# Kernel tuning notes

Measured on AMD Instinct MI355X. Metric: run time of the kernel, lower is better.

Reference implementation:

```python
import jax, jax.numpy as jnp
import numpy as np

C = 256      # in_channels
CI = 128     # inter_channels = in_channels // 2
B, H, W = 16, 64, 64
EPS = 1e-5   # BatchNorm2d default eps


def conv1x1(x, w, b=None):
    # x: (b,c,h,w), w: (o,c) -> (b,o,h,w)
    out = jnp.einsum('bchw,oc->bohw', x, w)
    if b is not None:
        out = out + b[None, :, None, None]
    return out


def maxpool2x2(x):
    b, c, h, w = x.shape
    return x.reshape(b, c, h // 2, 2, w // 2, 2).max(axis=(3, 5))


def setup_inputs() -> dict:
    key = jax.random.key(0)
    ks = jax.random.split(key, 12)
    s_in = 1.0 / np.sqrt(C)
    s_int = 1.0 / np.sqrt(CI)
    return {
        'x': jax.random.normal(ks[0], (B, C, H, W), jnp.float32),
        'y': jax.random.normal(ks[1], (B, C, H, W), jnp.float32),
        'theta_w': jax.random.uniform(ks[2], (CI, C), jnp.float32, -s_in, s_in),
        'theta_b': jax.random.uniform(ks[3], (CI,), jnp.float32, -s_in, s_in),
        'phi_w': jax.random.uniform(ks[4], (CI, C), jnp.float32, -s_in, s_in),
        'phi_b': jax.random.uniform(ks[5], (CI,), jnp.float32, -s_in, s_in),
        'g_w': jax.random.uniform(ks[6], (CI, C), jnp.float32, -s_in, s_in),
        'g_b': jax.random.uniform(ks[7], (CI,), jnp.float32, -s_in, s_in),
        'W_w': jax.random.uniform(ks[8], (C, CI), jnp.float32, -s_int, s_int),
        'W_b': jax.random.uniform(ks[9], (C,), jnp.float32, -s_int, s_int),
        'bn_gamma': jax.random.normal(ks[10], (C,), jnp.float32) * 0.1,
        'bn_beta': jax.random.normal(ks[11], (C,), jnp.float32) * 0.1,
    }


def reference(x, y, theta_w, theta_b, phi_w, phi_b, g_w, g_b, W_w, W_b, bn_gamma, bn_beta):
    b, c, h, w = x.shape
    # g branch: 1x1 conv on y + 2x2 maxpool -> (b, CI, hw/4) -> (b, hw/4, CI)
    g_y = maxpool2x2(conv1x1(y, g_w, g_b)).reshape(b, CI, -1).transpose(0, 2, 1)
    # theta branch: 1x1 conv on x -> (b, hw, CI)
    theta_x = conv1x1(x, theta_w, theta_b).reshape(b, CI, -1).transpose(0, 2, 1)
    # phi branch: 1x1 conv on y + maxpool -> (b, CI, hw/4)
    phi_y = maxpool2x2(conv1x1(y, phi_w, phi_b)).reshape(b, CI, -1)
    # attention: (b, hw, hw/4)
    f = jnp.einsum('bnc,bcm->bnm', theta_x, phi_y)
    f_div_C = jax.nn.softmax(f, axis=-1)
    # z: (b, hw, CI) -> (b, CI, h, w)
    z = jnp.einsum('bnm,bmc->bnc', f_div_C, g_y)
    z = z.transpose(0, 2, 1).reshape(b, CI, h, w)
    # W: 1x1 conv + BatchNorm2d (training-mode batch stats, biased var)
    wz = conv1x1(z, W_w, W_b)
    mean = wz.mean(axis=(0, 2, 3), keepdims=True)
    var = wz.var(axis=(0, 2, 3), keepdims=True)
    wz = (wz - mean) * jax.lax.rsqrt(var + EPS)
    wz = wz * bn_gamma[None, :, None, None] + bn_beta[None, :, None, None]
    return wz + x
```

## Files before the change

### kernel.cpp

```cpp
#include <hip/hip_runtime.h>
#include <cstdint>

#define HW 4096
#define NC 256
#define CI 128
#define NB 16
#define MP 1024

typedef __bf16 bfv8 __attribute__((ext_vector_type(8)));
typedef float f32x16 __attribute__((ext_vector_type(16)));

__device__ __forceinline__ uint32_t bfr(float x) {
    uint32_t u = __float_as_uint(x);
    return (u + 0x7fffu + ((u >> 16) & 1u)) >> 16;
}
__device__ __forceinline__ uint32_t pkbf(float a, float b) {
    return bfr(a) | (bfr(b) << 16);
}
__device__ __forceinline__ float b2f_lo(uint32_t u) { return __uint_as_float(u << 16); }
__device__ __forceinline__ float b2f_hi(uint32_t u) { return __uint_as_float(u & 0xffff0000u); }

__global__ void k_castw(const float* __restrict__ a, const float* __restrict__ b,
                        const float* __restrict__ c, const float* __restrict__ d,
                        ushort* __restrict__ dst) {
    const float* srcs[4] = {a, b, c, d};
    const float* s = srcs[blockIdx.y];
    int i = (blockIdx.x * 256 + threadIdx.x) * 8;
    float4 v0 = *(const float4*)(s + i);
    float4 v1 = *(const float4*)(s + i + 4);
    uint4 o;
    o.x = pkbf(v0.x, v0.y); o.y = pkbf(v0.z, v0.w);
    o.z = pkbf(v1.x, v1.y); o.w = pkbf(v1.z, v1.w);
    *(uint4*)(dst + (size_t)blockIdx.y * 32768 + i) = o;
}

template<int O_TILE, int NT>
__global__ __launch_bounds__(256) void k_conv_mfma(
        const float* __restrict__ in, const ushort* __restrict__ wbf,
        const float* __restrict__ bias0, const float* __restrict__ bias1,
        ushort* __restrict__ outT) {
    __shared__ ushort xs[NT * 256];
    const int t = threadIdx.x;
    constexpr int tilesPerB = 4096 / NT;
    const int b = blockIdx.x / tilesPerB;
    const int n0 = (blockIdx.x % tilesPerB) * NT;
    const float* inb = in + ((size_t)b * 256) * 4096 + n0;

    constexpr int RPP = 1024 / NT;
    const int c0 = t % RPP, q = t / RPP;
    #pragma unroll
    for (int p = 0; p < 256 / RPP; p++) {
        int c = c0 + p * RPP;
        float4 v = *(const float4*)(inb + (size_t)c * 4096 + q * 4);
        #pragma unroll
        for (int j = 0; j < 4; j++) {
            int n = q * 4 + j;
            xs[n * 256 + (c ^ ((n & 7) << 3))] = (ushort)bfr((&v.x)[j]);
        }
    }
    __syncthreads();

    const int lane = t & 63, w = t >> 6;
    const int ln = lane & 31, hi = lane >> 5;
    int ob0, nb0;
    if (O_TILE == 256) { ob0 = w * 2; nb0 = 0; }
    else               { ob0 = (w & 1) * 2; nb0 = (w >> 1) * 2; }

    f32x16 acc[2][2];
    #pragma unroll
    for (int i = 0; i < 2; i++)
        #pragma unroll
        for (int j = 0; j < 2; j++)
            #pragma unroll
            for (int k = 0; k < 16; k++) acc[i][j][k] = 0.f;

    const ushort* wr0 = wbf + (size_t)(ob0 * 32 + ln) * 256 + hi * 8;
    const ushort* wr1 = wr0 + 32 * 256;
    const int nr0 = nb0 * 32 + ln, nr1 = nr0 + 32;
    const int sw0 = (nr0 & 7) << 3, sw1 = (nr1 & 7) << 3;

    #pragma unroll 4
    for (int ks = 0; ks < 16; ks++) {
        int k = ks * 16 + hi * 8;
        bfv8 wf0 = *(const bfv8*)(wr0 + ks * 16);
        bfv8 wf1 = *(const bfv8*)(wr1 + ks * 16);
        bfv8 x0 = *(const bfv8*)&xs[nr0 * 256 + (k ^ sw0)];
        bfv8 x1 = *(const bfv8*)&xs[nr1 * 256 + (k ^ sw1)];
        acc[0][0] = __builtin_amdgcn_mfma_f32_32x32x16_bf16(wf0, x0, acc[0][0], 0, 0, 0);
        acc[0][1] = __builtin_amdgcn_mfma_f32_32x32x16_bf16(wf0, x1, acc[0][1], 0, 0, 0);
        acc[1][0] = __builtin_amdgcn_mfma_f32_32x32x16_bf16(wf1, x0, acc[1][0], 0, 0, 0);
        acc[1][1] = __builtin_amdgcn_mfma_f32_32x32x16_bf16(wf1, x1, acc[1][1], 0, 0, 0);
    }

    #pragma unroll
    for (int oi = 0; oi < 2; oi++) {
        int obb = (ob0 + oi) * 32;
        #pragma unroll
        for (int grp = 0; grp < 4; grp++) {
            int og = obb + grp * 8 + hi * 4;
            const float* bp = (O_TILE == 256 && og >= 128) ? bias1 : bias0;
            float4 bv = *(const float4*)&bp[og & 127];
            #pragma unroll
            for (int ni = 0; ni < 2; ni++) {
                int n = n0 + (nb0 + ni) * 32 + ln;
                float r0 = acc[oi][ni][grp * 4 + 0] + bv.x;
                float r1 = acc[oi][ni][grp * 4 + 1] + bv.y;
                float r2 = acc[oi][ni][grp * 4 + 2] + bv.z;
                float r3 = acc[oi][ni][grp * 4 + 3] + bv.w;
                uint2 pk;
                pk.x = pkbf(r0, r1); pk.y = pkbf(r2, r3);
                *(uint2*)&outT[((size_t)b * 4096 + n) * O_TILE + og] = pk;
            }
        }
    }
}

__global__ __launch_bounds__(256) void k_pool(const ushort* __restrict__ phig,
        ushort* __restrict__ phiT, ushort* __restrict__ gout) {
    __shared__ ushort gt[128][33];
    int b = blockIdx.x >> 5, ph = blockIdx.x & 31;
    int t = threadIdx.x;
    int c8 = (t & 31) * 8, pg = t >> 5;
    const ushort* base = phig + ((size_t)b * 4096) * 256;
    #pragma unroll
    for (int i = 0; i < 4; i++) {
        int pw = pg * 4 + i;
        int m = ph * 32 + pw;
        int n00 = 128 * ph + 2 * pw;
        uint4 a = *(const uint4*)(base + (size_t)(n00) * 256 + c8);
        uint4 bb = *(const uint4*)(base + (size_t)(n00 + 1) * 256 + c8);
        uint4 cc = *(const uint4*)(base + (size_t)(n00 + 64) * 256 + c8);
        uint4 dd = *(const uint4*)(base + (size_t)(n00 + 65) * 256 + c8);
        uint4 o;
        const uint32_t* pa = &a.x; const uint32_t* pbp = &bb.x;
        const uint32_t* pc = &cc.x; const uint32_t* pd = &dd.x;
        uint32_t* po = &o.x;
        #pragma unroll
        for (int k = 0; k < 4; k++) {
            float lo = fmaxf(fmaxf(b2f_lo(pa[k]), b2f_lo(pbp[k])), fmaxf(b2f_lo(pc[k]), b2f_lo(pd[k])));
            float hi = fmaxf(fmaxf(b2f_hi(pa[k]), b2f_hi(pbp[k])), fmaxf(b2f_hi(pc[k]), b2f_hi(pd[k])));
            po[k] = (__float_as_uint(lo) >> 16) | (__float_as_uint(hi) & 0xffff0000u);
        }
        if (c8 < 128) {
            *(uint4*)&phiT[((size_t)b * MP + m) * CI + c8] = o;
        } else {
            int c = c8 - 128;
            #pragma unroll
            for (int j = 0; j < 8; j++) {
                uint32_t word = po[j >> 1];
                gt[c + j][pw] = (j & 1) ? (ushort)(word >> 16) : (ushort)(word & 0xffffu);
            }
        }
    }
    __syncthreads();
    {
        int c = t >> 1, half = t & 1;
        ushort* grow = gout + ((size_t)b * CI + c) * MP + ph * 32 + half * 16;
        uint32_t wv[8];
        #pragma unroll
        for (int k = 0; k < 8; k++) {
            wv[k] = (uint32_t)gt[c][half * 16 + 2 * k] | ((uint32_t)gt[c][half * 16 + 2 * k + 1] << 16);
        }
        *(uint4*)grow = make_uint4(wv[0], wv[1], wv[2], wv[3]);
        *(uint4*)(grow + 8) = make_uint4(wv[4], wv[5], wv[6], wv[7]);
    }
}

__global__ __launch_bounds__(512, 2) void k_attn_mfma(
        const ushort* __restrict__ thetaT, const ushort* __restrict__ phiT,
        const ushort* __restrict__ gmat, ushort* __restrict__ zout) {
    __shared__ char lds[65536];
    const int t = threadIdx.x;
    const int w = t >> 6, lane = t & 63;
    const int nq = lane & 31, hi = lane >> 5;
    const int ngrp = w & 3, h = w >> 2;
    const int b = blockIdx.x >> 5;
    const int q0 = (blockIdx.x & 31) << 7;

    {
        int row = t >> 2, s0 = (t & 3) * 4;
        const uint4* src = (const uint4*)(thetaT + ((size_t)b * HW + q0 + row) * CI) + s0;
        uint4* dstrow = (uint4*)(lds + row * 256);
        int rsw = row & 15;
        #pragma unroll
        for (int j = 0; j < 4; j++) {
            uint4 v = src[j];
            dstrow[(s0 + j) ^ rsw] = v;
        }
    }
    __syncthreads();
    bfv8 qf[8];
    {
        int row = ngrp * 32 + nq;
        int rsw = row & 15;
        #pragma unroll
        for (int ks = 0; ks < 8; ks++) {
            qf[ks] = *(const bfv8*)(lds + row * 256 + (((ks * 2 + hi) ^ rsw) << 4));
        }
    }
    __syncthreads();

    f32x16 zacc[4];
    #pragma unroll
    for (int ct = 0; ct < 4; ct++)
        #pragma unroll
        for (int i = 0; i < 16; i++) zacc[ct][i] = 0.f;
    float run_sum = 0.f;

    const int reg_r = t >> 7, tt = t & 127;
    const int hh = reg_r >> 1, kind = reg_r & 1;

    const char* phiB = lds + h * 32768;
    const char* gB   = lds + h * 32768 + 16384;
    const int rswp = nq & 15;
    const int rswg = nq & 7;

    for (int it = 0; it < 8; it++) {
        if (kind == 0) {
            int row = tt >> 1, s0 = (tt & 1) * 8;
            const uint4* src = (const uint4*)(phiT + ((size_t)b * MP + hh * 512 + it * 64 + row) * CI) + s0;
            uint4* dstrow = (uint4*)(lds + hh * 32768 + row * 256);
            int rsw = row & 15;
            #pragma unroll
            for (int j = 0; j < 8; j++) {
                uint4 v = src[j];
                dstrow[(s0 + j) ^ rsw] = v;
            }
        } else {
            int row = tt;
            const uint4* src = (const uint4*)(gmat + ((size_t)b * CI + row) * MP + hh * 512 + it * 64);
            uint4* dstrow = (uint4*)(lds + hh * 32768 + 16384 + row * 128);
            int rsw = row & 7;
            #pragma unroll
            for (int j = 0; j < 8; j++) {
                uint4 v = src[j];
                dstrow[j ^ rsw] = v;
            }
        }
        __syncthreads();

        f32x16 sA, sB;
        #pragma unroll
        for (int i = 0; i < 16; i++) { sA[i] = 0.f; sB[i] = 0.f; }
        __builtin_amdgcn_s_setprio(1);
        #pragma unroll
        for (int ks = 0; ks < 8; ks++) {
            int slot = ks * 2 + hi;
            bfv8 a0 = *(const bfv8*)(phiB + nq * 256 + ((slot ^ rswp) << 4));
            bfv8 a1 = *(const bfv8*)(phiB + (32 + nq) * 256 + ((slot ^ rswp) << 4));
            sA = __builtin_amdgcn_mfma_f32_32x32x16_bf16(a0, qf[ks], sA, 0, 0, 0);
            sB = __builtin_amdgcn_mfma_f32_32x32x16_bf16(a1, qf[ks], sB, 0, 0, 0);
        }
        __builtin_amdgcn_s_setprio(0);

        float pA[16], pB[16];
        #pragma unroll
        for (int i = 0; i < 16; i++) { pA[i] = __expf(sA[i]); run_sum += pA[i]; }
        #pragma unroll
        for (int i = 0; i < 16; i++) { pB[i] = __expf(sB[i]); run_sum += pB[i]; }

        uint32_t wA[8], wB[8], tA[8], tB[8];
        #pragma unroll
        for (int j = 0; j < 8; j++) { wA[j] = pkbf(pA[2 * j], pA[2 * j + 1]); wB[j] = pkbf(pB[2 * j], pB[2 * j + 1]); }
        #pragma unroll
        for (int j = 0; j < 8; j++) { tA[j] = (uint32_t)__shfl_xor((int)wA[j], 32, 64); tB[j] = (uint32_t)__shfl_xor((int)wB[j], 32, 64); }
        bool lo = (hi == 0);
        union PU { uint32_t u[4]; bfv8 v; } p0A, p1A, p0B, p1B;
        p0A.u[0] = lo ? wA[0] : tA[2]; p0A.u[1] = lo ? wA[1] : tA[3];
        p0A.u[2] = lo ? tA[0] : wA[2]; p0A.u[3] = lo ? tA[1] : wA[3];
        p1A.u[0] = lo ? wA[4] : tA[6]; p1A.u[1] = lo ? wA[5] : tA[7];
        p1A.u[2] = lo ? tA[4] : wA[6]; p1A.u[3] = lo ? tA[5] : wA[7];
        p0B.u[0] = lo ? wB[0] : tB[2]; p0B.u[1] = lo ? wB[1] : tB[3];
        p0B.u[2] = lo ? tB[0] : wB[2]; p0B.u[3] = lo ? tB[1] : wB[3];
        p1B.u[0] = lo ? wB[4] : tB[6]; p1B.u[1] = lo ? wB[5] : tB[7];
        p1B.u[2] = lo ? tB[4] : wB[6]; p1B.u[3] = lo ? tB[5] : wB[7];

        __builtin_amdgcn_s_setprio(1);
        #pragma unroll
        for (int ct = 0; ct < 4; ct++) {
            const char* grow = gB + (ct * 32 + nq) * 128;
            bfv8 g0 = *(const bfv8*)(grow + (((0 * 2 + hi) ^ rswg) << 4));
            bfv8 g1 = *(const bfv8*)(grow + (((1 * 2 + hi) ^ rswg) << 4));
            bfv8 g2 = *(const bfv8*)(grow + (((2 * 2 + hi) ^ rswg) << 4));
            bfv8 g3 = *(const bfv8*)(grow + (((3 * 2 + hi) ^ rswg) << 4));
            zacc[ct] = __builtin_amdgcn_mfma_f32_32x32x16_bf16(g0, p0A.v, zacc[ct], 0, 0, 0);
            zacc[ct] = __builtin_amdgcn_mfma_f32_32x32x16_bf16(g1, p1A.v, zacc[ct], 0, 0, 0);
            zacc[ct] = __builtin_amdgcn_mfma_f32_32x32x16_bf16(g2, p0B.v, zacc[ct], 0, 0, 0);
            zacc[ct] = __builtin_amdgcn_mfma_f32_32x32x16_bf16(g3, p1B.v, zacc[ct], 0, 0, 0);
        }
        __builtin_amdgcn_s_setprio(0);
        __syncthreads();
    }

    float pair_sum = run_sum + __shfl_xor(run_sum, 32, 64);
    float* ssum = (float*)(lds + 32768);
    if (hi == 0) ssum[w * 32 + nq] = pair_sum;
    __syncthreads();
    float psum = ssum[(w ^ 4) * 32 + nq];
    float rinv = 1.f / (pair_sum + psum);

    ushort* zr = zout + ((size_t)b * HW + q0 + ngrp * 32 + nq) * CI;
    const int rswz = nq & 15;
    #pragma unroll
    for (int pass = 0; pass < 2; pass++) {
        __syncthreads();
        if (h == 1) {
            #pragma unroll
            for (int cth = 0; cth < 2; cth++) {
                int ct = pass * 2 + cth;
                #pragma unroll
                for (int grp = 0; grp < 4; grp++) {
                    int slot = cth * 8 + grp * 2 + hi;
                    float4 v;
                    v.x = zacc[ct][grp * 4 + 0];
                    v.y = zacc[ct][grp * 4 + 1];
                    v.z = zacc[ct][grp * 4 + 2];
                    v.w = zacc[ct][grp * 4 + 3];
                    *(float4*)(lds + ngrp * 8192 + nq * 256 + ((slot ^ rswz) << 4)) = v;
                }
            }
        }
        __syncthreads();
        if (h == 0) {
            #pragma unroll
            for (int cth = 0; cth < 2; cth++) {
                int ct = pass * 2 + cth;
                #pragma unroll
                for (int grp = 0; grp < 4; grp++) {
                    int slot = cth * 8 + grp * 2 + hi;
                    float4 pv = *(const float4*)(lds + ngrp * 8192 + nq * 256 + ((slot ^ rswz) << 4));
                    float v0 = (zacc[ct][grp * 4 + 0] + pv.x) * rinv;
                    float v1 = (zacc[ct][grp * 4 + 1] + pv.y) * rinv;
                    float v2 = (zacc[ct][grp * 4 + 2] + pv.z) * rinv;
                    float v3 = (zacc[ct][grp * 4 + 3] + pv.w) * rinv;
                    int c0 = ct * 32 + grp * 8 + hi * 4;
                    uint2 pk;
                    pk.x = pkbf(v0, v1);
                    pk.y = pkbf(v2, v3);
                    *(uint2*)(zr + c0) = pk;
                }
            }
        }
    }
}

__global__ __launch_bounds__(256) void k_wz_mfma(
        const ushort* __restrict__ z, const ushort* __restrict__ Wbf,
        const float* __restrict__ Wb, float* __restrict__ out,
        float* __restrict__ part) {
    __shared__ ushort zs[128 * 128];
    int t = threadIdx.x;
    int mtile = blockIdx.x;
    int oh = blockIdx.y;
    int b = mtile >> 5;
    int n0 = (mtile & 31) << 7;
    const ushort* zt = z + ((size_t)b * 4096 + n0) * 128;
    #pragma unroll
    for (int it = 0; it < 8; it++) {
        int d = (it * 256 + t) * 16;
        uint4 v = *(const uint4*)((const char*)zt + d);
        int n = d >> 8;
        int widx = (n << 7) + (((d & 255) ^ ((n & 7) << 4)) >> 1);
        *(uint4*)&zs[widx] = v;
    }
    __syncthreads();
    int lane = t & 63, w = t >> 6;
    int ln = lane & 31, hi = lane >> 5;
    int wr = w >> 1, wc = w & 1;
    f32x16 acc[2][2];
    #pragma unroll
    for (int i = 0; i < 2; i++)
        #pragma unroll
        for (int j = 0; j < 2; j++)
            #pragma unroll
            for (int k = 0; k < 16; k++) acc[i][j][k] = 0.f;
    const ushort* w0 = Wbf + (size_t)(oh * 128 + wc * 64 + ln) * 128 + hi * 8;
    const ushort* w1 = w0 + 32 * 128;
    int nr0 = wr * 64 + ln, nr1 = nr0 + 32;
    int sw0 = (nr0 & 7) << 3, sw1 = (nr1 & 7) << 3;
    #pragma unroll
    for (int ks = 0; ks < 8; ks++) {
        int k = ks * 16 + hi * 8;
        bfv8 a0 = *(const bfv8*)&zs[(nr0 << 7) + (k ^ sw0)];
        bfv8 a1 = *(const bfv8*)&zs[(nr1 << 7) + (k ^ sw1)];
        bfv8 b0 = *(const bfv8*)(w0 + ks * 16);
        bfv8 b1 = *(const bfv8*)(w1 + ks * 16);
        acc[0][0] = __builtin_amdgcn_mfma_f32_32x32x16_bf16(a0, b0, acc[0][0], 0, 0, 0);
        acc[0][1] = __builtin_amdgcn_mfma_f32_32x32x16_bf16(a0, b1, acc[0][1], 0, 0, 0);
        acc[1][0] = __builtin_amdgcn_mfma_f32_32x32x16_bf16(a1, b0, acc[1][0], 0, 0, 0);
        acc[1][1] = __builtin_amdgcn_mfma_f32_32x32x16_bf16(a1, b1, acc[1][1], 0, 0, 0);
    }
    #pragma unroll
    for (int obi = 0; obi < 2; obi++) {
        int o = oh * 128 + wc * 64 + obi * 32 + ln;
        float bv = Wb[o];
        float* orow = out + ((size_t)b * 256 + o) * 4096 + n0;
        float s = 0.f, qq = 0.f;
        #pragma unroll
        for (int nbi = 0; nbi < 2; nbi++) {
            #pragma unroll
            for (int grp = 0; grp < 4; grp++) {
                float4 vv;
                #pragma unroll
                for (int j = 0; j < 4; j++) {
                    float v = acc[nbi][obi][grp * 4 + j] + bv;
                    (&vv.x)[j] = v;
                    s += v; qq += v * v;
                }
                int n = (wr * 2 + nbi) * 32 + grp * 8 + hi * 4;
                *(float4*)(orow + n) = vv;
            }
        }
        s += __shfl_xor(s, 32, 64);
        qq += __shfl_xor(qq, 32, 64);
        if (hi == 0) {
            float* pr = part + (size_t)(mtile * 2 + wr) * 512;
            pr[o] = s;
            pr[256 + o] = qq;
        }
    }
}

__global__ __launch_bounds__(256) void k_bnstats(const float* __restrict__ part,
        const float* __restrict__ gamma, const float* __restrict__ beta,
        float* __restrict__ ss) {
    int o = blockIdx.x, t = threadIdx.x;
    float s = 0.f, q = 0.f;
    for (int k = t; k < 1024; k += 256) {
        s += part[(size_t)k * 512 + o];
        q += part[(size_t)k * 512 + 256 + o];
    }
    #pragma unroll
    for (int d = 32; d > 0; d >>= 1) { s += __shfl_down(s, d, 64); q += __shfl_down(q, d, 64); }
    __shared__ float rs[4], rq[4];
    int wave = t >> 6, lane = t & 63;
    if (lane == 0) { rs[wave] = s; rq[wave] = q; }
    __syncthreads();
    if (t == 0) {
        float S = rs[0] + rs[1] + rs[2] + rs[3];
        float Q = rq[0] + rq[1] + rq[2] + rq[3];
        const float inv = 1.0f / 65536.0f;
        float mean = S * inv;
        float var = Q * inv - mean * mean;
        float sc = gamma[o] * rsqrtf(var + 1e-5f);
        ss[o] = sc;
        ss[NC + o] = beta[o] - mean * sc;
    }
}

__global__ void k_apply(float* __restrict__ out, const float* __restrict__ x,
        const float* __restrict__ ss) {
    size_t i4 = (size_t)blockIdx.x * 256 + threadIdx.x;
    int o = (int)((i4 >> 10) & 255);
    float sc = ss[o], sh = ss[NC + o];
    float4 w = ((float4*)out)[i4];
    float4 xv = ((const float4*)x)[i4];
    float4 r;
    r.x = w.x * sc + sh + xv.x;
    r.y = w.y * sc + sh + xv.y;
    r.z = w.z * sc + sh + xv.z;
    r.w = w.w * sc + sh + xv.w;
    ((float4*)out)[i4] = r;
}

extern "C" void kernel_launch(void* const* d_in, const int* in_sizes, int n_in,
                              void* d_out, int out_size, void* d_ws, size_t ws_size,
                              hipStream_t stream) {
    const float* x       = (const float*)d_in[0];
    const float* y       = (const float*)d_in[1];
    const float* theta_w = (const float*)d_in[2];
    const float* theta_b = (const float*)d_in[3];
    const float* phi_w   = (const float*)d_in[4];
    const float* phi_b   = (const float*)d_in[5];
    const float* g_w     = (const float*)d_in[6];
    const float* g_b     = (const float*)d_in[7];
    const float* W_w     = (const float*)d_in[8];
    const float* W_b     = (const float*)d_in[9];
    const float* bn_g    = (const float*)d_in[10];
    const float* bn_b    = (const float*)d_in[11];
    float* ws  = (float*)d_ws;
    float* out = (float*)d_out;

    ushort* wbf    = (ushort*)ws;
    ushort* thetaT = (ushort*)(ws + 65536);
    ushort* phig   = (ushort*)(ws + 4259840);
    ushort* zbuf   = phig;
    ushort* phiT   = (ushort*)(ws + 12648448);
    ushort* gbuf   = (ushort*)(ws + 13697024);
    float*  part   = ws + 14745600;
    float*  ss     = ws + 15269888;

    k_castw<<<dim3(16, 4), 256, 0, stream>>>(theta_w, phi_w, g_w, W_w, wbf);

    k_conv_mfma<128, 128><<<NB * 32, 256, 0, stream>>>(x, wbf, theta_b, theta_b, thetaT);
    k_conv_mfma<256, 64><<<NB * 64, 256, 0, stream>>>(y, wbf + 32768, phi_b, g_b, phig);

    k_pool<<<NB * 32, 256, 0, stream>>>(phig, phiT, gbuf);

    k_attn_mfma<<<NB * 32, 512, 0, stream>>>(thetaT, phiT, gbuf, zbuf);

    k_wz_mfma<<<dim3(NB * 32, 2), 256, 0, stream>>>(zbuf, wbf + 98304, W_b, out, part);
    k_bnstats<<<256, 256, 0, stream>>>(part, bn_g, bn_b, ss);
    k_apply<<<16384, 256, 0, stream>>>(out, x, ss);
}
```

Measured before the change: 211.2 us.

## Store pre-BN conv output as bf16 and prefetch attention tiles across iterations

The W-conv kernel now writes its pre-normalisation output as bf16 into a workspace buffer rather than fp32 into the output, and the final apply kernel reads that bf16 buffer plus x and writes fp32. This halves the intermediate write and read traffic between the two kernels, at the cost of bf16 rounding before batch-norm (the statistics are still computed in fp32). The attention kernel also issues the first half of the next iteration's phi/g global loads after the barrier so they overlap with the MFMA compute. The z buffer is moved to a separate workspace region so it does not alias the new bf16 output buffer.

```diff
diff --git a/kernel.cpp b/kernel.cpp
--- a/kernel.cpp
+++ b/kernel.cpp
@@ -215,29 +215,48 @@
     const int rswp = nq & 15;
     const int rswg = nq & 7;
 
-    for (int it = 0; it < 8; it++) {
+    auto ldaddr = [&](int it, int j) -> const uint4* {
         if (kind == 0) {
             int row = tt >> 1, s0 = (tt & 1) * 8;
-            const uint4* src = (const uint4*)(phiT + ((size_t)b * MP + hh * 512 + it * 64 + row) * CI) + s0;
-            uint4* dstrow = (uint4*)(lds + hh * 32768 + row * 256);
-            int rsw = row & 15;
-            #pragma unroll
-            for (int j = 0; j < 8; j++) {
-                uint4 v = src[j];
-                dstrow[(s0 + j) ^ rsw] = v;
-            }
+            return (const uint4*)(phiT + ((size_t)b * MP + hh * 512 + it * 64 + row) * CI) + s0 + j;
         } else {
             int row = tt;
-            const uint4* src = (const uint4*)(gmat + ((size_t)b * CI + row) * MP + hh * 512 + it * 64);
-            uint4* dstrow = (uint4*)(lds + hh * 32768 + 16384 + row * 128);
-            int rsw = row & 7;
-            #pragma unroll
-            for (int j = 0; j < 8; j++) {
-                uint4 v = src[j];
-                dstrow[j ^ rsw] = v;
+            return (const uint4*)(gmat + ((size_t)b * CI + row) * MP + hh * 512 + it * 64) + j;
+        }
+    };
+
+    uint4 pf[4];
+    #pragma unroll
+    for (int j = 0; j < 4; j++) pf[j] = *ldaddr(0, j);
+
+    for (int it = 0; it < 8; it++) {
+        {
+            uint4 rest[4];
+            #pragma unroll
+            for (int j = 0; j < 4; j++) rest[j] = *ldaddr(it, 4 + j);
+            if (kind == 0) {
+                int row = tt >> 1, s0 = (tt & 1) * 8;
+                uint4* dstrow = (uint4*)(lds + hh * 32768 + row * 256);
+                int rsw = row & 15;
+                #pragma unroll
+                for (int j = 0; j < 4; j++) dstrow[(s0 + j) ^ rsw] = pf[j];
+                #pragma unroll
+                for (int j = 0; j < 4; j++) dstrow[(s0 + 4 + j) ^ rsw] = rest[j];
+            } else {
+                int row = tt;
+                uint4* dstrow = (uint4*)(lds + hh * 32768 + 16384 + row * 128);
+                int rsw = row & 7;
+                #pragma unroll
+                for (int j = 0; j < 4; j++) dstrow[j ^ rsw] = pf[j];
+                #pragma unroll
+                for (int j = 0; j < 4; j++) dstrow[(4 + j) ^ rsw] = rest[j];
             }
         }
         __syncthreads();
+        if (it < 7) {
+            #pragma unroll
+            for (int j = 0; j < 4; j++) pf[j] = *ldaddr(it + 1, j);
+        }
 
         f32x16 sA, sB;
         #pragma unroll
@@ -346,7 +365,7 @@
 
 __global__ __launch_bounds__(256) void k_wz_mfma(
         const ushort* __restrict__ z, const ushort* __restrict__ Wbf,
-        const float* __restrict__ Wb, float* __restrict__ out,
+        const float* __restrict__ Wb, ushort* __restrict__ wz,
         float* __restrict__ part) {
     __shared__ ushort zs[128 * 128];
     int t = threadIdx.x;
@@ -394,21 +413,24 @@
     for (int obi = 0; obi < 2; obi++) {
         int o = oh * 128 + wc * 64 + obi * 32 + ln;
         float bv = Wb[o];
-        float* orow = out + ((size_t)b * 256 + o) * 4096 + n0;
+        ushort* orow = wz + ((size_t)b * 256 + o) * 4096 + n0;
         float s = 0.f, qq = 0.f;
         #pragma unroll
         for (int nbi = 0; nbi < 2; nbi++) {
             #pragma unroll
             for (int grp = 0; grp < 4; grp++) {
-                float4 vv;
+                float vals[4];
                 #pragma unroll
                 for (int j = 0; j < 4; j++) {
                     float v = acc[nbi][obi][grp * 4 + j] + bv;
-                    (&vv.x)[j] = v;
+                    vals[j] = v;
                     s += v; qq += v * v;
                 }
                 int n = (wr * 2 + nbi) * 32 + grp * 8 + hi * 4;
-                *(float4*)(orow + n) = vv;
+                uint2 pk;
+                pk.x = pkbf(vals[0], vals[1]);
+                pk.y = pkbf(vals[2], vals[3]);
+                *(uint2*)(orow + n) = pk;
             }
         }
         s += __shfl_xor(s, 32, 64);
@@ -448,19 +470,25 @@
     }
 }
 
-__global__ void k_apply(float* __restrict__ out, const float* __restrict__ x,
-        const float* __restrict__ ss) {
-    size_t i4 = (size_t)blockIdx.x * 256 + threadIdx.x;
-    int o = (int)((i4 >> 10) & 255);
+__global__ void k_apply(float* __restrict__ out, const ushort* __restrict__ wz,
+        const float* __restrict__ x, const float* __restrict__ ss) {
+    size_t i = ((size_t)blockIdx.x * 256 + threadIdx.x) * 8;
+    int o = (int)((i >> 12) & 255);
     float sc = ss[o], sh = ss[NC + o];
-    float4 w = ((float4*)out)[i4];
-    float4 xv = ((const float4*)x)[i4];
-    float4 r;
-    r.x = w.x * sc + sh + xv.x;
-    r.y = w.y * sc + sh + xv.y;
-    r.z = w.z * sc + sh + xv.z;
-    r.w = w.w * sc + sh + xv.w;
-    ((float4*)out)[i4] = r;
+    uint4 wv = *(const uint4*)(wz + i);
+    float4 x0 = *(const float4*)(x + i);
+    float4 x1 = *(const float4*)(x + i + 4);
+    float4 r0, r1;
+    r0.x = b2f_lo(wv.x) * sc + sh + x0.x;
+    r0.y = b2f_hi(wv.x) * sc + sh + x0.y;
+    r0.z = b2f_lo(wv.y) * sc + sh + x0.z;
+    r0.w = b2f_hi(wv.y) * sc + sh + x0.w;
+    r1.x = b2f_lo(wv.z) * sc + sh + x1.x;
+    r1.y = b2f_hi(wv.z) * sc + sh + x1.y;
+    r1.z = b2f_lo(wv.w) * sc + sh + x1.z;
+    r1.w = b2f_hi(wv.w) * sc + sh + x1.w;
+    *(float4*)(out + i) = r0;
+    *(float4*)(out + i + 4) = r1;
 }
 
 extern "C" void kernel_launch(void* const* d_in, const int* in_sizes, int n_in,
@@ -483,8 +511,9 @@
 
     ushort* wbf    = (ushort*)ws;
     ushort* thetaT = (ushort*)(ws + 65536);
+    ushort* wzbf   = (ushort*)(ws + 65536);
     ushort* phig   = (ushort*)(ws + 4259840);
-    ushort* zbuf   = phig;
+    ushort* zbuf   = (ushort*)(ws + 8454144);
     ushort* phiT   = (ushort*)(ws + 12648448);
     ushort* gbuf   = (ushort*)(ws + 13697024);
     float*  part   = ws + 14745600;
@@ -499,7 +528,7 @@
 
     k_attn_mfma<<<NB * 32, 512, 0, stream>>>(thetaT, phiT, gbuf, zbuf);
 
-    k_wz_mfma<<<dim3(NB * 32, 2), 256, 0, stream>>>(zbuf, wbf + 98304, W_b, out, part);
+    k_wz_mfma<<<dim3(NB * 32, 2), 256, 0, stream>>>(zbuf, wbf + 98304, W_b, wzbf, part);
     k_bnstats<<<256, 256, 0, stream>>>(part, bn_g, bn_b, ss);
-    k_apply<<<16384, 256, 0, stream>>>(out, x, ss);
-}
+    k_apply<<<8192, 256, 0, stream>>>(out, wzbf, x, ss);
+}
```

New measurement: 259.8 us. +23.0%, slower.
